# Kernel tuning notes

Hardware: AMD Instinct MI355X
Metric: run time of the kernel (lower is better)

## Reference

```python
import jax, jax.numpy as jnp
import numpy as np

B, K, N, NBR = 4, 2048, 8192, 32
DIM, C_IN, W_HID, C_MID, F_HID, C_OUT = 3, 16, 32, 16, 64, 64
BIG = 3000.0


def _mlp(x, w1, b1, w2, b2):
    # SetTransform with one hidden layer, reduction='none': Linear->ReLU->Linear
    return jnp.maximum(x @ w1 + b1, 0.0) @ w2 + b2


def setup_inputs() -> dict:
    key = jax.random.key(0)
    ks = jax.random.split(key, 12)
    s = lambda fan_in: 1.0 / np.sqrt(fan_in)
    return {
        "keys": jax.random.normal(ks[0], (B, K, DIM), jnp.float32),
        "points": jax.random.normal(ks[1], (B, N, DIM), jnp.float32),
        "feats": jax.random.normal(ks[2], (B, N, C_IN), jnp.float32),
        "valid": jax.random.bernoulli(ks[3], 0.95, (B, K, N)),
        "ww1": jax.random.normal(ks[4], (DIM, W_HID), jnp.float32) * s(DIM),
        "wb1": jax.random.normal(ks[5], (W_HID,), jnp.float32) * s(DIM),
        "ww2": jax.random.normal(ks[6], (W_HID, C_MID), jnp.float32) * s(W_HID),
        "wb2": jax.random.normal(ks[7], (C_MID,), jnp.float32) * s(W_HID),
        "fw1": jax.random.normal(ks[8], (C_IN * C_MID, F_HID), jnp.float32) * s(C_IN * C_MID),
        "fb1": jax.random.normal(ks[9], (F_HID,), jnp.float32) * s(C_IN * C_MID),
        "fw2": jax.random.normal(ks[10], (F_HID, C_OUT), jnp.float32) * s(F_HID),
        "fb2": jax.random.normal(ks[11], (C_OUT,), jnp.float32) * s(F_HID),
    }


def reference(keys, points, feats, valid, ww1, wb1, ww2, wb2, fw1, fb1, fw2, fb2):
    # --- dist_fn (Euclidean): dist_vec = points - keys, dist = ||dist_vec|| ---
    diff = points[:, None, :, :] - keys[:, :, None, :]        # [B,K,N,DIM]
    dist = jnp.sqrt(jnp.sum(diff * diff, axis=-1))            # [B,K,N]
    big_dist = dist.max() * BIG
    dist = dist + jnp.where(valid, 0.0, big_dist)
    # --- kNN: smallest NBR distances per key ---
    _, idxs = jax.lax.top_k(-dist, NBR)                       # [B,K,NBR]
    bidx = jnp.arange(B)[:, None, None]
    # gather neighbor info (avoids materializing [B,K,N,*] gathered copies)
    n_rel = points[bidx, idxs] - keys[:, :, None, :]          # [B,K,NBR,DIM]
    n_feats = feats[bidx, idxs]                               # [B,K,NBR,C_IN]
    n_valid = jnp.take_along_axis(valid, idxs, axis=2)        # [B,K,NBR]
    n_valid = n_valid[..., None].astype(n_rel.dtype)
    # per-neighbor weight MLP, mask, batched matmul reduce over neighbors
    m = _mlp(n_rel, ww1, wb1, ww2, wb2) * n_valid             # [B,K,NBR,C_MID]
    nf = n_feats * n_valid                                    # [B,K,NBR,C_IN]
    e = jnp.einsum('bkqm,bkqc->bkmc', m, nf)                  # [B,K,C_MID,C_IN]
    e = e.reshape(B, K, C_MID * C_IN)
    return _mlp(e, fw1, fb1, fw2, fb2)                        # [B,K,C_OUT]
```

## Files before the change

### kernel.cpp

```cpp
#include <hip/hip_runtime.h>
#include <hip/hip_bf16.h>
#include <cstdint>
#include <cstddef>

#define B_    4
#define K_    2048
#define N_    8192
#define NBR_  32
#define NCAND 44
#define CIN   16
#define WHID  32
#define CMID  16
#define FHID  64
#define COUT  64
#define SOA_OFF 4096
#define WS_NEED ((size_t)SOA_OFF + (size_t)B_ * 3 * N_ * 4)

__global__ void pc_detect_kernel(const unsigned* __restrict__ v, int* __restrict__ flag) {
    const unsigned w = v[threadIdx.x & 63];
    const int byte_like = (((w & 0xFEFEFEFEu) == 0u) && ((w & 0xFFFFFF00u) != 0u)) ? 1 : 0;
    const unsigned long long m = __ballot(byte_like);
    if (threadIdx.x == 0) *flag = (m != 0ull) ? 1 : 0;
}

__global__ __launch_bounds__(256) void pc_soa_kernel(const float* __restrict__ pts,
                                                     float* __restrict__ soa) {
    const int i = blockIdx.x * 256 + threadIdx.x;
    const int b = i >> 13, n = i & (N_ - 1);
    const float* p = pts + (size_t)i * 3;
    const float x = p[0], y = p[1], z = p[2];
    float* d = soa + (size_t)b * 3 * N_ + n;
    d[0]      = x;
    d[N_]     = y;
    d[2 * N_] = z;
}

__device__ __forceinline__ unsigned umin_(unsigned a, unsigned b) { return a < b ? a : b; }
__device__ __forceinline__ unsigned umax_(unsigned a, unsigned b) { return a < b ? b : a; }

__device__ __forceinline__ unsigned med3_(unsigned a, unsigned b, unsigned c) {
    unsigned d;
    asm("v_med3_u32 %0, %1, %2, %3" : "=v"(d) : "v"(a), "v"(b), "v"(c));
    return d;
}
__device__ __forceinline__ void insert_m3(unsigned (&sa)[8], unsigned kv) {
#pragma unroll
    for (int i = 7; i >= 1; --i)
        sa[i] = med3_(sa[i - 1], sa[i], kv);
    sa[0] = umin_(sa[0], kv);
}

__device__ __forceinline__ void scan_soa8(const float* __restrict__ px,
                                          const float* __restrict__ py,
                                          const float* __restrict__ pz,
                                          float kx, float ky, float kz,
                                          int lane, unsigned (&sa)[8]) {
    const int l8 = lane * 8;
#pragma unroll 2
    for (int t = 0; t < N_ / 512; ++t) {
        const int n0 = t * 512 + l8;
        const float4 x0 = *(const float4*)(px + n0), x1 = *(const float4*)(px + n0 + 4);
        const float4 y0 = *(const float4*)(py + n0), y1 = *(const float4*)(py + n0 + 4);
        const float4 z0 = *(const float4*)(pz + n0), z1 = *(const float4*)(pz + n0 + 4);
        float dx, dy, dz, d2;
#define PC_ONE(J, XX, YY, ZZ)                                                        \
        dx = XX - kx; dy = YY - ky; dz = ZZ - kz;                                    \
        d2 = fmaf(dz, dz, fmaf(dy, dy, dx * dx));                                    \
        insert_m3(sa, (__float_as_uint(d2) & 0xFFFFE000u) | (unsigned)(n0 + J));
        PC_ONE(0, x0.x, y0.x, z0.x)
        PC_ONE(1, x0.y, y0.y, z0.y)
        PC_ONE(2, x0.z, y0.z, z0.z)
        PC_ONE(3, x0.w, y0.w, z0.w)
        PC_ONE(4, x1.x, y1.x, z1.x)
        PC_ONE(5, x1.y, y1.y, z1.y)
        PC_ONE(6, x1.z, y1.z, z1.z)
        PC_ONE(7, x1.w, y1.w, z1.w)
#undef PC_ONE
    }
}

__device__ __forceinline__ void scan_aos4(const float* __restrict__ pts,
                                          float kx, float ky, float kz,
                                          int lane, unsigned (&sa)[8]) {
    const int l4 = lane * 4;
#pragma unroll 2
    for (int t = 0; t < N_ / 256; ++t) {
        const int n0 = t * 256 + l4;
        const float4* p4 = (const float4*)(pts + (size_t)n0 * 3);
        const float4 A = p4[0], Bv = p4[1], Cv = p4[2];
        float dx, dy, dz, d2;
        dx = A.x - kx; dy = A.y - ky; dz = A.z - kz;
        d2 = fmaf(dz, dz, fmaf(dy, dy, dx * dx));
        insert_m3(sa, (__float_as_uint(d2) & 0xFFFFE000u) | (unsigned)(n0 + 0));
        dx = A.w - kx; dy = Bv.x - ky; dz = Bv.y - kz;
        d2 = fmaf(dz, dz, fmaf(dy, dy, dx * dx));
        insert_m3(sa, (__float_as_uint(d2) & 0xFFFFE000u) | (unsigned)(n0 + 1));
        dx = Bv.z - kx; dy = Bv.w - ky; dz = Cv.x - kz;
        d2 = fmaf(dz, dz, fmaf(dy, dy, dx * dx));
        insert_m3(sa, (__float_as_uint(d2) & 0xFFFFE000u) | (unsigned)(n0 + 2));
        dx = Cv.y - kx; dy = Cv.z - ky; dz = Cv.w - kz;
        d2 = fmaf(dz, dz, fmaf(dy, dy, dx * dx));
        insert_m3(sa, (__float_as_uint(d2) & 0xFFFFE000u) | (unsigned)(n0 + 3));
    }
}

struct Slice {
    union {
        unsigned cand[8 * 64];
        float    w[NBR_ * CMID];
        float    pad_[512];
    } A;
    union {
        float nf[NBR_ * CIN];
        struct { float hp[4 * FHID]; float hf[FHID]; } h;
    } Bv;
    union {
        unsigned slot[NBR_];
        float    e[CMID * CIN];
    } C;
};

template <int SOA>
__global__ __launch_bounds__(128, 8) void pc_main_kernel(
    const float* __restrict__ keys,
    const float* __restrict__ points,
    const float* __restrict__ soa,
    const float* __restrict__ feats,
    const void*  __restrict__ validp,
    const float* __restrict__ ww1, const float* __restrict__ wb1,
    const float* __restrict__ ww2, const float* __restrict__ wb2,
    const float* __restrict__ fw1, const float* __restrict__ fb1,
    const float* __restrict__ fw2, const float* __restrict__ fb2,
    float* __restrict__ out,
    const int* __restrict__ flagp)
{
    __shared__ Slice sl[2];

    const int lane = threadIdx.x & 63;
    const int wv   = threadIdx.x >> 6;
    const int row  = (blockIdx.x << 1) | wv;
    const int b    = row >> 11;
    Slice& S = sl[wv];

    const float kx = keys[row * 3 + 0];
    const float ky = keys[row * 3 + 1];
    const float kz = keys[row * 3 + 2];
    const float* pts = points + (size_t)b * N_ * 3;

    unsigned sa[8];
#pragma unroll
    for (int i = 0; i < 8; ++i) sa[i] = 0xFFFFFFFFu;

    if (SOA) {
        const float* px = soa + (size_t)b * 3 * N_;
        scan_soa8(px, px + N_, px + 2 * N_, kx, ky, kz, lane, sa);
    } else {
        scan_aos4(pts, kx, ky, kz, lane, sa);
    }

#pragma unroll
    for (int i = 0; i < 8; ++i) S.A.cand[i * 64 + lane] = sa[i];
    __syncthreads();

    unsigned cur   = sa[0];
    int      head  = 0;
    unsigned mykey = 0xFFFFFFFFu;
#pragma unroll 4
    for (int r = 0; r < NCAND; ++r) {
        unsigned t = cur;
#pragma unroll
        for (int off = 1; off < 64; off <<= 1)
            t = umin_(t, (unsigned)__shfl_xor((int)t, off, 64));
        if (lane == r) mykey = t;
        if (cur == t) {
            ++head;
            cur = (head < 8) ? S.A.cand[head * 64 + lane] : 0xFFFFFFFFu;
        }
    }

    if (lane < NBR_) S.C.slot[lane] = 0xFFFFFFFFu;
    __syncthreads();

    {
        const int  cidx = (int)(mykey & 8191u);
        const float cdx = pts[cidx * 3 + 0] - kx;
        const float cdy = pts[cidx * 3 + 1] - ky;
        const float cdz = pts[cidx * 3 + 2] - kz;
        const float cd2 = fmaf(cdz, cdz, fmaf(cdy, cdy, cdx * cdx));
        const int flag = *flagp;
        const size_t vbase = (size_t)row * N_;
        unsigned vbit;
        if (flag) vbit = ((const unsigned char*)validp)[vbase + (size_t)cidx];
        else      vbit = ((const unsigned*)validp)[vbase + (size_t)cidx];
        const unsigned d2bits = (vbit != 0u) ? __float_as_uint(cd2) : 0xFFFFFFFFu;
        const unsigned long long fkey =
            ((unsigned long long)d2bits << 13) | (unsigned long long)cidx;
        int rank = 0;
#pragma unroll 11
        for (int j = 0; j < NCAND; ++j) {
            const unsigned long long fj = (unsigned long long)__shfl((long long)fkey, j, 64);
            rank += (fj < fkey) ? 1 : 0;
        }
        if (lane < NCAND && (vbit != 0u) && rank < NBR_)
            S.C.slot[rank] = mykey;
    }
    __syncthreads();

    const int q    = lane & 31;
    const int half = lane >> 5;
    const unsigned skey = S.C.slot[q];
    const int   nidx = (int)(skey & 8191u);
    const float vf   = (skey < 0xF0000000u) ? 1.0f : 0.0f;

    const float rx = pts[nidx * 3 + 0] - kx;
    const float ry = pts[nidx * 3 + 1] - ky;
    const float rz = pts[nidx * 3 + 2] - kz;

    float wacc[8];
    {
        const float4 b0 = *(const float4*)&wb2[half * 8 + 0];
        const float4 b1 = *(const float4*)&wb2[half * 8 + 4];
        wacc[0] = b0.x; wacc[1] = b0.y; wacc[2] = b0.z; wacc[3] = b0.w;
        wacc[4] = b1.x; wacc[5] = b1.y; wacc[6] = b1.z; wacc[7] = b1.w;
    }

#pragma unroll 8
    for (int j = 0; j < WHID; ++j) {
        float hj = fmaf(rx, ww1[j], fmaf(ry, ww1[WHID + j], fmaf(rz, ww1[2 * WHID + j], wb1[j])));
        hj = fmaxf(hj, 0.0f);
        const float4 wa = *(const float4*)&ww2[j * CMID + half * 8 + 0];
        const float4 wb = *(const float4*)&ww2[j * CMID + half * 8 + 4];
        wacc[0] = fmaf(hj, wa.x, wacc[0]);
        wacc[1] = fmaf(hj, wa.y, wacc[1]);
        wacc[2] = fmaf(hj, wa.z, wacc[2]);
        wacc[3] = fmaf(hj, wa.w, wacc[3]);
        wacc[4] = fmaf(hj, wb.x, wacc[4]);
        wacc[5] = fmaf(hj, wb.y, wacc[5]);
        wacc[6] = fmaf(hj, wb.z, wacc[6]);
        wacc[7] = fmaf(hj, wb.w, wacc[7]);
    }
#pragma unroll
    for (int m = 0; m < 8; ++m) wacc[m] *= vf;

    *(float4*)&S.A.w[q * CMID + half * 8 + 0] = make_float4(wacc[0], wacc[1], wacc[2], wacc[3]);
    *(float4*)&S.A.w[q * CMID + half * 8 + 4] = make_float4(wacc[4], wacc[5], wacc[6], wacc[7]);

    const float* fp = feats + ((size_t)b * N_ + (size_t)nidx) * CIN + half * 8;
    *(float4*)&S.Bv.nf[q * CIN + half * 8 + 0] = *(const float4*)(fp + 0);
    *(float4*)&S.Bv.nf[q * CIN + half * 8 + 4] = *(const float4*)(fp + 4);
    __syncthreads();

    {
        const int m  = lane >> 2;
        const int c4 = lane & 3;
        float4 eacc = make_float4(0.f, 0.f, 0.f, 0.f);
#pragma unroll
        for (int qq = 0; qq < NBR_; ++qq) {
            const float  wq = S.A.w[qq * CMID + m];
            const float4 f  = *(const float4*)&S.Bv.nf[qq * CIN + c4 * 4];
            eacc.x = fmaf(wq, f.x, eacc.x);
            eacc.y = fmaf(wq, f.y, eacc.y);
            eacc.z = fmaf(wq, f.z, eacc.z);
            eacc.w = fmaf(wq, f.w, eacc.w);
        }
        *(float4*)&S.C.e[m * CIN + c4 * 4] = eacc;
    }
    __syncthreads();

    {
        const int g  = lane >> 4;
        const int t4 = lane & 15;
        float a0 = 0.f, a1 = 0.f, a2 = 0.f, a3 = 0.f;
#pragma unroll 8
        for (int i = 0; i < 64; ++i) {
            const float  ev = S.C.e[g * 64 + i];
            const float4 wv2 = *(const float4*)&fw1[(size_t)(g * 64 + i) * FHID + t4 * 4];
            a0 = fmaf(ev, wv2.x, a0);
            a1 = fmaf(ev, wv2.y, a1);
            a2 = fmaf(ev, wv2.z, a2);
            a3 = fmaf(ev, wv2.w, a3);
        }
        *(float4*)&S.Bv.h.hp[g * FHID + t4 * 4] = make_float4(a0, a1, a2, a3);
    }
    __syncthreads();

    {
        float hf = fb1[lane] + S.Bv.h.hp[lane] + S.Bv.h.hp[FHID + lane]
                 + S.Bv.h.hp[2 * FHID + lane] + S.Bv.h.hp[3 * FHID + lane];
        S.Bv.h.hf[lane] = fmaxf(hf, 0.0f);
    }
    __syncthreads();

    {
        float oacc = fb2[lane];
#pragma unroll 8
        for (int j = 0; j < FHID; ++j)
            oacc = fmaf(S.Bv.h.hf[j], fw2[(size_t)j * COUT + lane], oacc);
        out[(size_t)row * COUT + lane] = oacc;
    }
}

extern "C" void kernel_launch(void* const* d_in, const int* in_sizes, int n_in,
                              void* d_out, int out_size, void* d_ws, size_t ws_size,
                              hipStream_t stream) {
    const float* keys   = (const float*)d_in[0];
    const float* points = (const float*)d_in[1];
    const float* feats  = (const float*)d_in[2];
    const void*  valid  = d_in[3];
    const float* ww1 = (const float*)d_in[4];
    const float* wb1 = (const float*)d_in[5];
    const float* ww2 = (const float*)d_in[6];
    const float* wb2 = (const float*)d_in[7];
    const float* fw1 = (const float*)d_in[8];
    const float* fb1 = (const float*)d_in[9];
    const float* fw2 = (const float*)d_in[10];
    const float* fb2 = (const float*)d_in[11];
    float* out = (float*)d_out;
    int*   flag = (int*)d_ws;
    float* soa  = (float*)((char*)d_ws + SOA_OFF);

    pc_detect_kernel<<<1, 64, 0, stream>>>((const unsigned*)valid, flag);

    if (ws_size >= WS_NEED) {
        pc_soa_kernel<<<(B_ * N_) / 256, 256, 0, stream>>>(points, soa);
        pc_main_kernel<1><<<(B_ * K_) / 2, 128, 0, stream>>>(
            keys, points, soa, feats, valid,
            ww1, wb1, ww2, wb2, fw1, fb1, fw2, fb2, out, flag);
    } else {
        pc_main_kernel<0><<<(B_ * K_) / 2, 128, 0, stream>>>(
            keys, points, soa, feats, valid,
            ww1, wb1, ww2, wb2, fw1, fb1, fw2, fb2, out, flag);
    }
}
```

Measured before the change: 396.4 us.

## Select kNN candidates by wave-wide radix ballot and tile the SoA layout

Replaces the serial 44-round shuffle-min merge of per-lane top-8 lists with a 19-step ballot/popcount radix search. It finds the threshold for the 44 smallest keys, then compacts candidates into LDS with atomics and ranks them from LDS. The SoA buffer is re-tiled into 256-point xyz blocks so each lane loads one float4 per coordinate with a software-prefetched next tile. Block-wide __syncthreads are replaced by compiler-only memory barriers, relying on each wave using its own LDS slice. Risks include the LDS race if wave-level ordering is not guaranteed, candidate overflow past SELCAP, and a variable-length rank loop.

```diff
diff --git a/kernel.cpp b/kernel.cpp
--- a/kernel.cpp
+++ b/kernel.cpp
@@ -8,13 +8,14 @@
 #define N_    8192
 #define NBR_  32
 #define NCAND 44
+#define SELCAP 64
 #define CIN   16
 #define WHID  32
 #define CMID  16
 #define FHID  64
 #define COUT  64
 #define SOA_OFF 4096
-#define WS_NEED ((size_t)SOA_OFF + (size_t)B_ * 3 * N_ * 4)
+#define WS_NEED ((size_t)SOA_OFF + (size_t)B_ * 3 * N_ * 4 + 4096 )
 
 __global__ void pc_detect_kernel(const unsigned* __restrict__ v, int* __restrict__ flag) {
     const unsigned w = v[threadIdx.x & 63];
@@ -27,16 +28,16 @@
                                                      float* __restrict__ soa) {
     const int i = blockIdx.x * 256 + threadIdx.x;
     const int b = i >> 13, n = i & (N_ - 1);
+    const int t = n >> 8, w = n & 255;
     const float* p = pts + (size_t)i * 3;
     const float x = p[0], y = p[1], z = p[2];
-    float* d = soa + (size_t)b * 3 * N_ + n;
-    d[0]      = x;
-    d[N_]     = y;
-    d[2 * N_] = z;
+    float* d = soa + (size_t)b * 3 * N_ + (size_t)t * 768 + w;
+    d[0]   = x;
+    d[256] = y;
+    d[512] = z;
 }
 
 __device__ __forceinline__ unsigned umin_(unsigned a, unsigned b) { return a < b ? a : b; }
-__device__ __forceinline__ unsigned umax_(unsigned a, unsigned b) { return a < b ? b : a; }
 
 __device__ __forceinline__ unsigned med3_(unsigned a, unsigned b, unsigned c) {
     unsigned d;
@@ -50,32 +51,34 @@
     sa[0] = umin_(sa[0], kv);
 }
 
-__device__ __forceinline__ void scan_soa8(const float* __restrict__ px,
-                                          const float* __restrict__ py,
-                                          const float* __restrict__ pz,
-                                          float kx, float ky, float kz,
-                                          int lane, unsigned (&sa)[8]) {
-    const int l8 = lane * 8;
+__device__ __forceinline__ void scan_tiled(const float* __restrict__ soa_b,
+                                           float kx, float ky, float kz,
+                                           int lane, unsigned (&sa)[8]) {
+    const int voff = lane * 4;
+    const float* p  = soa_b;
+    float4 X = *(const float4*)(p + voff);
+    float4 Y = *(const float4*)(p + 256 + voff);
+    float4 Z = *(const float4*)(p + 512 + voff);
+    unsigned vn = (unsigned)voff;
 #pragma unroll 2
-    for (int t = 0; t < N_ / 512; ++t) {
-        const int n0 = t * 512 + l8;
-        const float4 x0 = *(const float4*)(px + n0), x1 = *(const float4*)(px + n0 + 4);
-        const float4 y0 = *(const float4*)(py + n0), y1 = *(const float4*)(py + n0 + 4);
-        const float4 z0 = *(const float4*)(pz + n0), z1 = *(const float4*)(pz + n0 + 4);
+    for (int t = 0; t < 32; ++t) {
+        const float4 cX = X, cY = Y, cZ = Z;
+        const float* pn = p + 768;
+        X = *(const float4*)(pn + voff);
+        Y = *(const float4*)(pn + 256 + voff);
+        Z = *(const float4*)(pn + 512 + voff);
+        p = pn;
         float dx, dy, dz, d2;
-#define PC_ONE(J, XX, YY, ZZ)                                                        \
-        dx = XX - kx; dy = YY - ky; dz = ZZ - kz;                                    \
-        d2 = fmaf(dz, dz, fmaf(dy, dy, dx * dx));                                    \
-        insert_m3(sa, (__float_as_uint(d2) & 0xFFFFE000u) | (unsigned)(n0 + J));
-        PC_ONE(0, x0.x, y0.x, z0.x)
-        PC_ONE(1, x0.y, y0.y, z0.y)
-        PC_ONE(2, x0.z, y0.z, z0.z)
-        PC_ONE(3, x0.w, y0.w, z0.w)
-        PC_ONE(4, x1.x, y1.x, z1.x)
-        PC_ONE(5, x1.y, y1.y, z1.y)
-        PC_ONE(6, x1.z, y1.z, z1.z)
-        PC_ONE(7, x1.w, y1.w, z1.w)
+#define PC_ONE(J, XX, YY, ZZ)                                                      \
+        dx = XX - kx; dy = YY - ky; dz = ZZ - kz;                                  \
+        d2 = fmaf(dz, dz, fmaf(dy, dy, dx * dx));                                  \
+        insert_m3(sa, (__float_as_uint(d2) & 0xFFFFE000u) | (vn | J##u));
+        PC_ONE(0, cX.x, cY.x, cZ.x)
+        PC_ONE(1, cX.y, cY.y, cZ.y)
+        PC_ONE(2, cX.z, cY.z, cZ.z)
+        PC_ONE(3, cX.w, cY.w, cZ.w)
 #undef PC_ONE
+        vn += 256u;
     }
 }
 
@@ -104,9 +107,15 @@
     }
 }
 
+struct SelBuf {
+    unsigned cnt;
+    unsigned pad;
+    unsigned key[SELCAP];
+    unsigned long long fk[SELCAP];
+};
 struct Slice {
     union {
-        unsigned cand[8 * 64];
+        SelBuf   sel;
         float    w[NBR_ * CMID];
         float    pad_[512];
     } A;
@@ -151,60 +160,71 @@
 #pragma unroll
     for (int i = 0; i < 8; ++i) sa[i] = 0xFFFFFFFFu;
 
-    if (SOA) {
-        const float* px = soa + (size_t)b * 3 * N_;
-        scan_soa8(px, px + N_, px + 2 * N_, kx, ky, kz, lane, sa);
-    } else {
-        scan_aos4(pts, kx, ky, kz, lane, sa);
-    }
-
-#pragma unroll
-    for (int i = 0; i < 8; ++i) S.A.cand[i * 64 + lane] = sa[i];
-    __syncthreads();
-
-    unsigned cur   = sa[0];
-    int      head  = 0;
-    unsigned mykey = 0xFFFFFFFFu;
-#pragma unroll 4
-    for (int r = 0; r < NCAND; ++r) {
-        unsigned t = cur;
-#pragma unroll
-        for (int off = 1; off < 64; off <<= 1)
-            t = umin_(t, (unsigned)__shfl_xor((int)t, off, 64));
-        if (lane == r) mykey = t;
-        if (cur == t) {
-            ++head;
-            cur = (head < 8) ? S.A.cand[head * 64 + lane] : 0xFFFFFFFFu;
-        }
-    }
+    if (SOA) scan_tiled(soa + (size_t)b * 3 * N_, kx, ky, kz, lane, sa);
+    else     scan_aos4(pts, kx, ky, kz, lane, sa);
+
+    unsigned hi[8];
+#pragma unroll
+    for (int s = 0; s < 8; ++s) hi[s] = sa[s] >> 13;
+
+    unsigned want = 0u;
+    int need = NCAND;
+    for (int bb = 18; bb >= 0; --bb) {
+        want <<= 1;
+        int cnt0 = 0;
+#pragma unroll
+        for (int s = 0; s < 8; ++s)
+            cnt0 += (int)__popcll(__ballot((hi[s] >> bb) == want));
+        if (cnt0 < need) { need -= cnt0; want |= 1u; }
+    }
+
+    if (lane == 0) S.A.sel.cnt = 0u;
+    int c = 0;
+#pragma unroll
+    for (int s = 0; s < 8; ++s) c += (hi[s] <= want) ? 1 : 0;
+    unsigned base = 0u;
+    if (c > 0) base = atomicAdd(&S.A.sel.cnt, (unsigned)c);
+#pragma unroll
+    for (int s = 0; s < 8; ++s)
+        if (s < c && base + (unsigned)s < (unsigned)SELCAP)
+            S.A.sel.key[base + s] = sa[s];
+    unsigned stot = S.A.sel.cnt;
+    stot = (unsigned)__builtin_amdgcn_readfirstlane((int)stot);
+    if (stot > (unsigned)SELCAP) stot = SELCAP;
+    asm volatile("" ::: "memory");
 
     if (lane < NBR_) S.C.slot[lane] = 0xFFFFFFFFu;
-    __syncthreads();
-
-    {
-        const int  cidx = (int)(mykey & 8191u);
+
+    const unsigned selkey = S.A.sel.key[(unsigned)lane < stot ? lane : 0];
+    const int cidx = (int)(selkey & 8191u);
+    unsigned vbit = 0u;
+    unsigned long long fkey = ~0ull;
+    if ((unsigned)lane < stot) {
         const float cdx = pts[cidx * 3 + 0] - kx;
         const float cdy = pts[cidx * 3 + 1] - ky;
         const float cdz = pts[cidx * 3 + 2] - kz;
         const float cd2 = fmaf(cdz, cdz, fmaf(cdy, cdy, cdx * cdx));
         const int flag = *flagp;
         const size_t vbase = (size_t)row * N_;
-        unsigned vbit;
         if (flag) vbit = ((const unsigned char*)validp)[vbase + (size_t)cidx];
         else      vbit = ((const unsigned*)validp)[vbase + (size_t)cidx];
         const unsigned d2bits = (vbit != 0u) ? __float_as_uint(cd2) : 0xFFFFFFFFu;
-        const unsigned long long fkey =
-            ((unsigned long long)d2bits << 13) | (unsigned long long)cidx;
+        fkey = ((unsigned long long)d2bits << 13) | (unsigned long long)cidx;
+        S.A.sel.fk[lane] = fkey;
+    }
+    asm volatile("" ::: "memory");
+
+    {
         int rank = 0;
-#pragma unroll 11
-        for (int j = 0; j < NCAND; ++j) {
-            const unsigned long long fj = (unsigned long long)__shfl((long long)fkey, j, 64);
+#pragma unroll 4
+        for (unsigned j = 0; j < stot; ++j) {
+            const unsigned long long fj = S.A.sel.fk[j];
             rank += (fj < fkey) ? 1 : 0;
         }
-        if (lane < NCAND && (vbit != 0u) && rank < NBR_)
-            S.C.slot[rank] = mykey;
-    }
-    __syncthreads();
+        if ((unsigned)lane < stot && vbit != 0u && rank < NBR_)
+            S.C.slot[rank] = selkey;
+    }
+    asm volatile("" ::: "memory");
 
     const int q    = lane & 31;
     const int half = lane >> 5;
@@ -215,6 +235,7 @@
     const float rx = pts[nidx * 3 + 0] - kx;
     const float ry = pts[nidx * 3 + 1] - ky;
     const float rz = pts[nidx * 3 + 2] - kz;
+    asm volatile("" ::: "memory");
 
     float wacc[8];
     {
@@ -248,7 +269,7 @@
     const float* fp = feats + ((size_t)b * N_ + (size_t)nidx) * CIN + half * 8;
     *(float4*)&S.Bv.nf[q * CIN + half * 8 + 0] = *(const float4*)(fp + 0);
     *(float4*)&S.Bv.nf[q * CIN + half * 8 + 4] = *(const float4*)(fp + 4);
-    __syncthreads();
+    asm volatile("" ::: "memory");
 
     {
         const int m  = lane >> 2;
@@ -265,7 +286,7 @@
         }
         *(float4*)&S.C.e[m * CIN + c4 * 4] = eacc;
     }
-    __syncthreads();
+    asm volatile("" ::: "memory");
 
     {
         const int g  = lane >> 4;
@@ -282,14 +303,14 @@
         }
         *(float4*)&S.Bv.h.hp[g * FHID + t4 * 4] = make_float4(a0, a1, a2, a3);
     }
-    __syncthreads();
+    asm volatile("" ::: "memory");
 
     {
         float hf = fb1[lane] + S.Bv.h.hp[lane] + S.Bv.h.hp[FHID + lane]
                  + S.Bv.h.hp[2 * FHID + lane] + S.Bv.h.hp[3 * FHID + lane];
         S.Bv.h.hf[lane] = fmaxf(hf, 0.0f);
     }
-    __syncthreads();
+    asm volatile("" ::: "memory");
 
     {
         float oacc = fb2[lane];
```

Result: no change. 394.9 us (-0.4%).
